# Optimization experiments

Measured on AMD Instinct MI355X. Metric: run time of the kernel, lower is better.

The kernel has to match this reference:

```python
import jax, jax.numpy as jnp
import numpy as np

N_COMBIN, N_DEV, CONT, VOCAB, EMB = 50000, 100000, 62, 1000, 16
B, K, H, OUT, NCLS = 8192, 64, 4, 16, 1
FEAT = CONT + 2 * EMB  # 94
ALPHA = 0.2  # leaky relu slope


def setup_inputs() -> dict:
    key = jax.random.key(0)
    ks = jax.random.split(key, 32)
    rn = lambda k, shape, s=0.05: (jax.random.normal(k, shape, dtype=jnp.float32) * s)
    inp = {
        "combin_cont": jax.random.normal(ks[0], (N_COMBIN, CONT), jnp.float32),
        "combin_cat": jax.random.randint(ks[1], (N_COMBIN, 2), 0, VOCAB),
        "device_cont": jax.random.normal(ks[2], (N_DEV, CONT), jnp.float32),
        "device_cat": jax.random.randint(ks[3], (N_DEV, 2), 0, VOCAB),
        "combin_idx": jax.random.randint(ks[4], (B,), 0, N_COMBIN),
        "device_idx": jax.random.randint(ks[5], (B,), 0, N_DEV),
        "neighbor_idx": jax.random.randint(ks[6], (B, K), 0, N_DEV),
        "ce0": rn(ks[7], (VOCAB, EMB), 1.0),
        "ce1": rn(ks[8], (VOCAB, EMB), 1.0),
        "de0": rn(ks[9], (VOCAB, EMB), 1.0),
        "de1": rn(ks[10], (VOCAB, EMB), 1.0),
        "Wc": rn(ks[11], (H, FEAT, OUT)),
        "bc": rn(ks[12], (H, OUT)),
        "Wd": rn(ks[13], (H, FEAT, OUT)),
        "bd": rn(ks[14], (H, OUT)),
        "aW": rn(ks[15], (H, 2 * OUT)),
        "ab": rn(ks[16], (H,)),
        "W1": rn(ks[17], (H * OUT, OUT)),
        "b1": rn(ks[18], (OUT,)),
        "W2": rn(ks[19], (OUT + 2 * FEAT, 64)),
        "b2": rn(ks[20], (64,)),
        "W3": rn(ks[21], (64, 32)),
        "b3": rn(ks[22], (32,)),
        "W4": rn(ks[23], (32, NCLS)),
        "b4": rn(ks[24], (NCLS,)),
    }
    return inp


def reference(combin_cont, combin_cat, device_cont, device_cat,
              combin_idx, device_idx, neighbor_idx,
              ce0, ce1, de0, de1,
              Wc, bc, Wd, bd, aW, ab,
              W1, b1, W2, b2, W3, b3, W4, b4):
    # concat_embed_feats for device nodes: [N_dev, FEAT]
    dev_feats = jnp.concatenate(
        [device_cont, de0[device_cat[:, 0]], de1[device_cat[:, 1]]], axis=1)
    # combin batch features: [B, FEAT]
    cc = combin_cat[combin_idx]
    comb_batch = jnp.concatenate(
        [combin_cont[combin_idx], ce0[cc[:, 0]], ce1[cc[:, 1]]], axis=1)
    dev_batch = dev_feats[device_idx]            # [B, FEAT]
    neibr = dev_feats[neighbor_idx]              # [B, K, FEAT]

    # multi-head GAT attention (all heads vectorized)
    h_c = jnp.einsum('bf,hfo->bho', comb_batch, Wc) + bc[None]          # [B,H,OUT]
    h_n = jnp.einsum('bkf,hfo->bhko', neibr, Wd) + bd[None, :, None]    # [B,H,K,OUT]
    a1, a2 = aW[:, :OUT], aW[:, OUT:]
    e = (jnp.einsum('bho,ho->bh', h_c, a1)[:, :, None]
         + jnp.einsum('bhko,ho->bhk', h_n, a2)
         + ab[None, :, None])                                           # [B,H,K]
    e = jax.nn.leaky_relu(e, negative_slope=ALPHA)
    attn = jax.nn.softmax(e, axis=-1)
    head_out = jax.nn.elu(jnp.einsum('bhk,bhko->bho', attn, h_n))       # [B,H,OUT]
    attn_feats = head_out.reshape(head_out.shape[0], H * OUT) @ W1 + b1  # [B,OUT]

    fusion = jnp.concatenate([comb_batch, dev_batch, attn_feats], axis=1)
    x = jax.nn.relu(fusion @ W2 + b2)   # dropout is identity in eval
    x = jax.nn.relu(x @ W3 + b3)
    return jax.nn.sigmoid(x @ W4 + b4)  # [B, NCLS]
```

## Files before the change

kernel.cpp:

```cpp
#include <hip/hip_runtime.h>
#include <cmath>

#define NDEV   100000
#define NBATCH 8192
#define CONTF  62
#define EMB    16
#define FEAT   94
#define KNBR   64
#define NH     4
#define OUTD   16
#define HOUT   64
#define FUS    204
#define ALPHA  0.2f

#define NDEVG2  782
#define NCOMBG2 64
#define KP      48
#define WROWS   68

typedef unsigned short ushortT;
typedef unsigned int   uintT;
typedef ushortT ushort8v __attribute__((ext_vector_type(8)));
typedef short   short8  __attribute__((ext_vector_type(8)));
typedef float   float4v __attribute__((ext_vector_type(4)));


template <typename T>
__device__ __forceinline__ const T* uniform_ptr(const T* p) {
  uint64_t v = (uint64_t)(uintptr_t)p;
  uint32_t lo = __builtin_amdgcn_readfirstlane((uint32_t)v);
  uint32_t hi = __builtin_amdgcn_readfirstlane((uint32_t)(v >> 32));
  return (const T*)(uintptr_t)(((uint64_t)hi << 32) | lo);
}

__device__ __forceinline__ float bf2f(ushortT u) {
  return __uint_as_float(((unsigned int)u) << 16);
}
__device__ __forceinline__ ushortT f2bf(float f) {
  unsigned int i = __float_as_uint(f);
  unsigned int r = i + 0x7FFFu + ((i >> 16) & 1u);
  return (ushortT)(r >> 16);
}
__device__ __forceinline__ uintT pack2(float lo, float hi) {
  return ((uintT)f2bf(hi) << 16) | (uintT)f2bf(lo);
}

union FragU { uint4 u; short8 s; };

__global__ __launch_bounds__(256) void k_prep(
    const float* __restrict__ Wd, const float* __restrict__ Wc,
    const float* __restrict__ aW,
    uintT* __restrict__ wpack) {
  const int e = blockIdx.x * 256 + threadIdx.x;
  if (e >= 2 * WROWS * KP) return;
  const bool dev = e < WROWS * KP;
  const int i = dev ? e : e - WROWS * KP;
  const int n = i / KP, p = i - n * KP;
  const float* __restrict__ Ws = dev ? Wd : Wc;
  uintT v = 0u;
  if (p < 47) {
    if (n < 64) {
      const int h = n >> 4, o = n & 15;
      const float lo = Ws[(h * FEAT + 2 * p) * OUTD + o];
      const float hi = Ws[(h * FEAT + 2 * p + 1) * OUTD + o];
      v = pack2(lo, hi);
    } else {
      const int hd = n - 64;
      const float* __restrict__ av = aW + hd * 2 * OUTD + (dev ? OUTD : 0);
      float lo = 0.f, hi = 0.f;
#pragma unroll
      for (int o = 0; o < OUTD; ++o) {
        lo = fmaf(Ws[(hd * FEAT + 2 * p) * OUTD + o], av[o], lo);
        hi = fmaf(Ws[(hd * FEAT + 2 * p + 1) * OUTD + o], av[o], hi);
      }
      v = pack2(lo, hi);
    }
  }
  wpack[e] = v;
}

__global__ __launch_bounds__(256, 2) void k_feat(
    const float* __restrict__ device_cont, const int* __restrict__ device_cat,
    const float* __restrict__ de0, const float* __restrict__ de1,
    const float* __restrict__ bd,
    const float* __restrict__ combin_cont, const int* __restrict__ combin_cat,
    const int* __restrict__ combin_idx,
    const float* __restrict__ ce0, const float* __restrict__ ce1,
    const float* __restrict__ bc,
    const float* __restrict__ aW, const uintT* __restrict__ wpack,
    ushortT* __restrict__ h_bf, float* __restrict__ e_d, float* __restrict__ e_c) {
  __shared__ uintT x_s[128 * KP];
  __shared__ uintT w_s[80 * KP];
  __shared__ int   ci_s[128];

  const int tid  = threadIdx.x;
  const int lane = tid & 63;
  const int wv = __builtin_amdgcn_readfirstlane((int)(tid >> 6));
  const int blk = blockIdx.x;
  const bool devp = blk < NDEVG2;
  const int b0 = (devp ? blk : blk - NDEVG2) * 128;

  if (!devp && tid < 128) ci_s[tid] = combin_idx[b0 + tid];

  {
    const uint4* __restrict__ wp =
        reinterpret_cast<const uint4*>(wpack + (devp ? 0 : WROWS * KP));
    uint4* __restrict__ ws4 = reinterpret_cast<uint4*>(w_s);
#pragma unroll
    for (int t = 0; t < 4; ++t) {
      const int idx = t * 256 + tid;
      if (idx < 960)
        ws4[idx] = (idx < 816) ? wp[idx] : make_uint4(0u, 0u, 0u, 0u);
    }
  }
  __syncthreads();

  {
    const float* __restrict__ cont = devp ? device_cont : combin_cont;
#pragma unroll 1
    for (int e = tid; e < 128 * 31; e += 256) {
      const int r = e / 31, p = e - r * 31;
      const size_t srow = devp ? (size_t)min(b0 + r, NDEV - 1) : (size_t)ci_s[r];
      const float2 v = *reinterpret_cast<const float2*>(cont + srow * CONTF + 2 * p);
      x_s[r * KP + p] = pack2(v.x, v.y);
    }
  }
  {
    const int r = tid >> 1, tb = tid & 1;
    const int srow = devp ? min(b0 + r, NDEV - 1) : ci_s[r];
    const int cidx = (devp ? device_cat : combin_cat)[2 * srow + tb];
    const float* __restrict__ ep =
        (tb ? (devp ? de1 : ce1) : (devp ? de0 : ce0)) + (size_t)cidx * EMB;
    uintT* __restrict__ dst = &x_s[r * KP + 31 + tb * 8];
#pragma unroll
    for (int k4 = 0; k4 < 4; ++k4) {
      const float4 v = reinterpret_cast<const float4*>(ep)[k4];
      dst[2 * k4 + 0] = pack2(v.x, v.y);
      dst[2 * k4 + 1] = pack2(v.z, v.w);
    }
  }
  if (tid < 128) x_s[tid * KP + 47] = 0u;
  __syncthreads();

  const int m = lane & 15, q = lane >> 4;
  const int aoff = devp ? OUTD : 0;
  const float* bias = uniform_ptr(devp ? bd : bc);
  const float* aWl  = uniform_ptr(aW);

  float4v acc[2][NH];
#pragma unroll
  for (int ct = 0; ct < NH; ++ct) {
    const float bv = bias[ct * OUTD + m];
    acc[0][ct] = (float4v){bv, bv, bv, bv};
    acc[1][ct] = (float4v){bv, bv, bv, bv};
  }
  float bec = 0.f;
  if (m < NH) {
    const float* __restrict__ av = aWl + m * 2 * OUTD + aoff;
#pragma unroll
    for (int o = 0; o < OUTD; ++o) bec = fmaf(bias[m * OUTD + o], av[o], bec);
  }
  float4v acc_e[2];
  acc_e[0] = (float4v){bec, bec, bec, bec};
  acc_e[1] = (float4v){bec, bec, bec, bec};

  const uintT* xa0 = &x_s[(wv * 16 + m) * KP + q * 4];
  const uintT* xa1 = &x_s[(64 + wv * 16 + m) * KP + q * 4];
#pragma unroll
  for (int c = 0; c < 3; ++c) {
    FragU af0, af1;
    af0.u = *reinterpret_cast<const uint4*>(xa0 + c * 16);
    af1.u = *reinterpret_cast<const uint4*>(xa1 + c * 16);
#pragma unroll
    for (int ct = 0; ct < NH; ++ct) {
      FragU bf;
      bf.u = *reinterpret_cast<const uint4*>(&w_s[(ct * 16 + m) * KP + c * 16 + q * 4]);
      acc[0][ct] = __builtin_amdgcn_mfma_f32_16x16x32_bf16(af0.s, bf.s, acc[0][ct], 0, 0, 0);
      acc[1][ct] = __builtin_amdgcn_mfma_f32_16x16x32_bf16(af1.s, bf.s, acc[1][ct], 0, 0, 0);
    }
    FragU bfe;
    bfe.u = *reinterpret_cast<const uint4*>(&w_s[(64 + m) * KP + c * 16 + q * 4]);
    acc_e[0] = __builtin_amdgcn_mfma_f32_16x16x32_bf16(af0.s, bfe.s, acc_e[0], 0, 0, 0);
    acc_e[1] = __builtin_amdgcn_mfma_f32_16x16x32_bf16(af1.s, bfe.s, acc_e[1], 0, 0, 0);
  }

  float* __restrict__ eout = devp ? e_d : e_c;
#pragma unroll
  for (int rt = 0; rt < 2; ++rt) {
    const int rowq = b0 + rt * 64 + wv * 16 + q * 4;
    if (m < NH) {
#pragma unroll
      for (int r = 0; r < 4; ++r)
        if (!devp || rowq + r < NDEV) eout[(size_t)(rowq + r) * NH + m] = acc_e[rt][r];
    }
    if (devp) {
#pragma unroll
      for (int ct = 0; ct < NH; ++ct) {
#pragma unroll
        for (int r = 0; r < 4; ++r) {
          if (rowq + r < NDEV)
            h_bf[(size_t)(rowq + r) * HOUT + ct * OUTD + m] = f2bf(acc[rt][ct][r]);
        }
      }
    }
  }
}

__global__ __launch_bounds__(256, 4) void k_attn(
    const int* __restrict__ neighbor_idx, const int* __restrict__ device_idx,
    const int* __restrict__ device_cat, const float* __restrict__ device_cont,
    const float* __restrict__ de0, const float* __restrict__ de1,
    const int* __restrict__ combin_idx, const int* __restrict__ combin_cat,
    const float* __restrict__ combin_cont,
    const float* __restrict__ ce0, const float* __restrict__ ce1,
    const ushortT* __restrict__ h_bf, const float* __restrict__ e_d,
    const float* __restrict__ e_c, const float* __restrict__ ab,
    const float* __restrict__ W1, const float* __restrict__ b1,
    const float* __restrict__ W2, const float* __restrict__ b2,
    const float* __restrict__ W3, const float* __restrict__ b3,
    const float* __restrict__ W4, const float* __restrict__ b4,
    float* __restrict__ out) {
  __shared__ __align__(16) float pb[4][NH][68];
  __shared__ __align__(16) float hb[4][HOUT];
  __shared__ __align__(16) float fusb[4][208];
  __shared__ __align__(16) float x1b[4][64];

  const int lane = threadIdx.x & 63;
  const int wid  = __builtin_amdgcn_readfirstlane((int)(threadIdx.x >> 6));
  const int b    = blockIdx.x * 4 + wid;

  const int nk = neighbor_idx[(size_t)b * KNBR + lane];
  const float4 ed4 = *reinterpret_cast<const float4*>(e_d + (size_t)nk * NH);
  const float4 ec4 = *reinterpret_cast<const float4*>(e_c + (size_t)b * NH);
  const float4 ab4 = *reinterpret_cast<const float4*>(ab);

  const int q = lane >> 3, c8 = lane & 7;
  ushort8v hpre[8];
#pragma unroll
  for (int t = 0; t < 8; ++t) {
    const int nt = __shfl(nk, q * 8 + t);
    hpre[t] = *reinterpret_cast<const ushort8v*>(h_bf + (size_t)nt * HOUT + c8 * 8);
  }

  const int ci = combin_idx[b];
  const int cc0 = combin_cat[2 * ci], cc1 = combin_cat[2 * ci + 1];
  const int didx = device_idx[b];
  const int dc0 = device_cat[2 * didx], dc1 = device_cat[2 * didx + 1];
#pragma unroll
  for (int t = 0; t < 3; ++t) {
    const int i = lane + t * 64;
    if (i < 188) {
      float v;
      if (i < 62)       v = combin_cont[(size_t)ci * CONTF + i];
      else if (i < 78)  v = ce0[(size_t)cc0 * EMB + (i - 62)];
      else if (i < 94)  v = ce1[(size_t)cc1 * EMB + (i - 78)];
      else if (i < 156) v = device_cont[(size_t)didx * CONTF + (i - 94)];
      else if (i < 172) v = de0[(size_t)dc0 * EMB + (i - 156)];
      else              v = de1[(size_t)dc1 * EMB + (i - 172)];
      fusb[wid][i] = v;
    }
  }

  float v0 = ec4.x + ed4.x + ab4.x;
  float v1 = ec4.y + ed4.y + ab4.y;
  float v2 = ec4.z + ed4.z + ab4.z;
  float v3 = ec4.w + ed4.w + ab4.w;
  v0 = v0 > 0.f ? v0 : ALPHA * v0;
  v1 = v1 > 0.f ? v1 : ALPHA * v1;
  v2 = v2 > 0.f ? v2 : ALPHA * v2;
  v3 = v3 > 0.f ? v3 : ALPHA * v3;

  float p0 = expf(v0), p1 = expf(v1), p2 = expf(v2), p3 = expf(v3);
  float s0 = p0, s1 = p1, s2 = p2, s3 = p3;
#pragma unroll
  for (int msk = 1; msk < 64; msk <<= 1) {
    s0 += __shfl_xor(s0, msk);
    s1 += __shfl_xor(s1, msk);
    s2 += __shfl_xor(s2, msk);
    s3 += __shfl_xor(s3, msk);
  }
  p0 /= s0; p1 /= s1; p2 /= s2; p3 /= s3;

  pb[wid][0][lane] = p0;
  pb[wid][1][lane] = p1;
  pb[wid][2][lane] = p2;
  pb[wid][3][lane] = p3;
  __builtin_amdgcn_wave_barrier();

  {
    const int hq = c8 >> 1;
    const float4 pA4 = *reinterpret_cast<const float4*>(&pb[wid][hq][q * 8]);
    const float4 pB4 = *reinterpret_cast<const float4*>(&pb[wid][hq][q * 8 + 4]);
    const float pv[8] = {pA4.x, pA4.y, pA4.z, pA4.w,
                         pB4.x, pB4.y, pB4.z, pB4.w};
    float a[8];
#pragma unroll
    for (int i = 0; i < 8; ++i) a[i] = 0.f;
#pragma unroll
    for (int t = 0; t < 8; ++t) {
      const float p = pv[t];
#pragma unroll
      for (int i = 0; i < 8; ++i) a[i] = fmaf(p, bf2f(hpre[t][i]), a[i]);
    }
#pragma unroll
    for (int msk = 8; msk < 64; msk <<= 1) {
#pragma unroll
      for (int i = 0; i < 8; ++i) a[i] += __shfl_xor(a[i], msk);
    }
    if (q == 0) {
#pragma unroll
      for (int i = 0; i < 8; ++i) a[i] = a[i] > 0.f ? a[i] : expm1f(a[i]);
      float4* hp = reinterpret_cast<float4*>(&hb[wid][c8 * 8]);
      hp[0] = make_float4(a[0], a[1], a[2], a[3]);
      hp[1] = make_float4(a[4], a[5], a[6], a[7]);
    }
  }
  __builtin_amdgcn_wave_barrier();

  {
    const int j = lane & 15, gg = lane >> 4;
    const float4* hv4 = reinterpret_cast<const float4*>(&hb[wid][gg * 16]);
    float pc0 = 0.f, pc1 = 0.f;
#pragma unroll
    for (int t4 = 0; t4 < 4; ++t4) {
      const float4 hv = hv4[t4];
      const int tb = gg * 16 + t4 * 4;
      pc0 = fmaf(hv.x, W1[(tb + 0) * OUTD + j], pc0);
      pc1 = fmaf(hv.y, W1[(tb + 1) * OUTD + j], pc1);
      pc0 = fmaf(hv.z, W1[(tb + 2) * OUTD + j], pc0);
      pc1 = fmaf(hv.w, W1[(tb + 3) * OUTD + j], pc1);
    }
    float part = pc0 + pc1;
    part += __shfl_xor(part, 16);
    part += __shfl_xor(part, 32);
    if (lane < 16) fusb[wid][188 + lane] = part + b1[lane];
  }
  __builtin_amdgcn_wave_barrier();

  {
    float a0 = b2[lane], a1 = 0.f, a2 = 0.f, a3 = 0.f;
    const float4* fu4 = reinterpret_cast<const float4*>(fusb[wid]);
#pragma unroll 3
    for (int f4 = 0; f4 < 51; ++f4) {
      const float4 u = fu4[f4];
      const int fb = f4 * 4;
      a0 = fmaf(u.x, W2[(fb + 0) * 64 + lane], a0);
      a1 = fmaf(u.y, W2[(fb + 1) * 64 + lane], a1);
      a2 = fmaf(u.z, W2[(fb + 2) * 64 + lane], a2);
      a3 = fmaf(u.w, W2[(fb + 3) * 64 + lane], a3);
    }
    x1b[wid][lane] = fmaxf((a0 + a1) + (a2 + a3), 0.f);
  }
  __builtin_amdgcn_wave_barrier();

  const int m = lane & 31, rh = lane >> 5;
  {
    float x2a = rh ? 0.f : b3[m], x2b = 0.f, x2c = 0.f, x2d = 0.f;
    const float4* xv4 = reinterpret_cast<const float4*>(&x1b[wid][rh * 32]);
#pragma unroll
    for (int j4 = 0; j4 < 8; ++j4) {
      const float4 xv = xv4[j4];
      const int jb = rh * 32 + j4 * 4;
      x2a = fmaf(xv.x, W3[(jb + 0) * 32 + m], x2a);
      x2b = fmaf(xv.y, W3[(jb + 1) * 32 + m], x2b);
      x2c = fmaf(xv.z, W3[(jb + 2) * 32 + m], x2c);
      x2d = fmaf(xv.w, W3[(jb + 3) * 32 + m], x2d);
    }
    float x2 = (x2a + x2b) + (x2c + x2d);
    x2 += __shfl_xor(x2, 32);
    float pL3 = fmaxf(x2, 0.f) * W4[m];
#pragma unroll
    for (int msk = 1; msk < 32; msk <<= 1) pL3 += __shfl_xor(pL3, msk);
    if (lane == 0) {
      const float z = pL3 + b4[0];
      out[b] = 1.f / (1.f + expf(-z));
    }
  }
}

extern "C" void kernel_launch(void* const* d_in, const int* in_sizes, int n_in,
                              void* d_out, int out_size, void* d_ws, size_t ws_size,
                              hipStream_t stream) {
  const float* combin_cont  = (const float*)d_in[0];
  const int*   combin_cat   = (const int*)d_in[1];
  const float* device_cont  = (const float*)d_in[2];
  const int*   device_cat   = (const int*)d_in[3];
  const int*   combin_idx   = (const int*)d_in[4];
  const int*   device_idx   = (const int*)d_in[5];
  const int*   neighbor_idx = (const int*)d_in[6];
  const float* ce0 = (const float*)d_in[7];
  const float* ce1 = (const float*)d_in[8];
  const float* de0 = (const float*)d_in[9];
  const float* de1 = (const float*)d_in[10];
  const float* Wc  = (const float*)d_in[11];
  const float* bc  = (const float*)d_in[12];
  const float* Wd  = (const float*)d_in[13];
  const float* bd  = (const float*)d_in[14];
  const float* aW  = (const float*)d_in[15];
  const float* ab  = (const float*)d_in[16];
  const float* W1  = (const float*)d_in[17];
  const float* b1  = (const float*)d_in[18];
  const float* W2  = (const float*)d_in[19];
  const float* b2  = (const float*)d_in[20];
  const float* W3  = (const float*)d_in[21];
  const float* b3  = (const float*)d_in[22];
  const float* W4  = (const float*)d_in[23];
  const float* b4  = (const float*)d_in[24];

  float* ws  = (float*)d_ws;
  ushortT* h_bf = (ushortT*)ws;
  float* e_d = ws + 3200000;
  float* e_c = ws + 3600000;
  uintT* wpack = (uintT*)(ws + 3632768);

  k_prep<<<26, 256, 0, stream>>>(Wd, Wc, aW, wpack);
  k_feat<<<NDEVG2 + NCOMBG2, 256, 0, stream>>>(
      device_cont, device_cat, de0, de1, bd,
      combin_cont, combin_cat, combin_idx, ce0, ce1, bc, aW, wpack,
      h_bf, e_d, e_c);
  k_attn<<<2048, 256, 0, stream>>>(
      neighbor_idx, device_idx, device_cat, device_cont, de0, de1,
      combin_idx, combin_cat, combin_cont, ce0, ce1,
      h_bf, e_d, e_c, ab, W1, b1, W2, b2, W3, b3, W4, b4, (float*)d_out);
}
```

Baseline: 162.2 us.

## Process two batch rows per wave in attention kernel; skip unused combin h MFMAs

The attention/MLP kernel now has each wave handle two batch rows instead of one. Weight loads for W1, W2 and W3 are shared across both rows, and the neighbor h gathers for both rows are issued together to raise memory-level parallelism. The grid is halved to match. Separately, the feature kernel skips the per-head h MFMAs for combin blocks, which only need the attention-score column. The cost is doubled register pressure from two hpre arrays, which could reduce occupancy under launch_bounds(256,4).

```diff
diff --git a/kernel.cpp b/kernel.cpp
--- a/kernel.cpp
+++ b/kernel.cpp
@@ -148,11 +148,13 @@
   const float* aWl  = uniform_ptr(aW);
 
   float4v acc[2][NH];
-#pragma unroll
-  for (int ct = 0; ct < NH; ++ct) {
-    const float bv = bias[ct * OUTD + m];
-    acc[0][ct] = (float4v){bv, bv, bv, bv};
-    acc[1][ct] = (float4v){bv, bv, bv, bv};
+  if (devp) {
+#pragma unroll
+    for (int ct = 0; ct < NH; ++ct) {
+      const float bv = bias[ct * OUTD + m];
+      acc[0][ct] = (float4v){bv, bv, bv, bv};
+      acc[1][ct] = (float4v){bv, bv, bv, bv};
+    }
   }
   float bec = 0.f;
   if (m < NH) {
@@ -171,12 +173,14 @@
     FragU af0, af1;
     af0.u = *reinterpret_cast<const uint4*>(xa0 + c * 16);
     af1.u = *reinterpret_cast<const uint4*>(xa1 + c * 16);
-#pragma unroll
-    for (int ct = 0; ct < NH; ++ct) {
-      FragU bf;
-      bf.u = *reinterpret_cast<const uint4*>(&w_s[(ct * 16 + m) * KP + c * 16 + q * 4]);
-      acc[0][ct] = __builtin_amdgcn_mfma_f32_16x16x32_bf16(af0.s, bf.s, acc[0][ct], 0, 0, 0);
-      acc[1][ct] = __builtin_amdgcn_mfma_f32_16x16x32_bf16(af1.s, bf.s, acc[1][ct], 0, 0, 0);
+    if (devp) {
+#pragma unroll
+      for (int ct = 0; ct < NH; ++ct) {
+        FragU bf;
+        bf.u = *reinterpret_cast<const uint4*>(&w_s[(ct * 16 + m) * KP + c * 16 + q * 4]);
+        acc[0][ct] = __builtin_amdgcn_mfma_f32_16x16x32_bf16(af0.s, bf.s, acc[0][ct], 0, 0, 0);
+        acc[1][ct] = __builtin_amdgcn_mfma_f32_16x16x32_bf16(af1.s, bf.s, acc[1][ct], 0, 0, 0);
+      }
     }
     FragU bfe;
     bfe.u = *reinterpret_cast<const uint4*>(&w_s[(64 + m) * KP + c * 16 + q * 4]);
@@ -220,160 +224,223 @@
     const float* __restrict__ W3, const float* __restrict__ b3,
     const float* __restrict__ W4, const float* __restrict__ b4,
     float* __restrict__ out) {
-  __shared__ __align__(16) float pb[4][NH][68];
-  __shared__ __align__(16) float hb[4][HOUT];
-  __shared__ __align__(16) float fusb[4][208];
-  __shared__ __align__(16) float x1b[4][64];
+  __shared__ __align__(16) float pb[8][NH][68];
+  __shared__ __align__(16) float hb[8][HOUT];
+  __shared__ __align__(16) float fusb[8][208];
+  __shared__ __align__(16) float x1b[8][64];
 
   const int lane = threadIdx.x & 63;
   const int wid  = __builtin_amdgcn_readfirstlane((int)(threadIdx.x >> 6));
-  const int b    = blockIdx.x * 4 + wid;
-
-  const int nk = neighbor_idx[(size_t)b * KNBR + lane];
-  const float4 ed4 = *reinterpret_cast<const float4*>(e_d + (size_t)nk * NH);
-  const float4 ec4 = *reinterpret_cast<const float4*>(e_c + (size_t)b * NH);
-  const float4 ab4 = *reinterpret_cast<const float4*>(ab);
+  const int row0 = blockIdx.x * 8 + wid * 2;
+  const int row1 = row0 + 1;
+  const int rl0  = wid * 2, rl1 = rl0 + 1;
+
+  const int nk0 = neighbor_idx[(size_t)row0 * KNBR + lane];
+  const int nk1 = neighbor_idx[(size_t)row1 * KNBR + lane];
+  const float4 ed40 = *reinterpret_cast<const float4*>(e_d + (size_t)nk0 * NH);
+  const float4 ed41 = *reinterpret_cast<const float4*>(e_d + (size_t)nk1 * NH);
+  const float4 ec40 = *reinterpret_cast<const float4*>(e_c + (size_t)row0 * NH);
+  const float4 ec41 = *reinterpret_cast<const float4*>(e_c + (size_t)row1 * NH);
+  const float4 ab4  = *reinterpret_cast<const float4*>(ab);
 
   const int q = lane >> 3, c8 = lane & 7;
-  ushort8v hpre[8];
+  ushort8v hpre0[8], hpre1[8];
 #pragma unroll
   for (int t = 0; t < 8; ++t) {
-    const int nt = __shfl(nk, q * 8 + t);
-    hpre[t] = *reinterpret_cast<const ushort8v*>(h_bf + (size_t)nt * HOUT + c8 * 8);
-  }
-
-  const int ci = combin_idx[b];
-  const int cc0 = combin_cat[2 * ci], cc1 = combin_cat[2 * ci + 1];
-  const int didx = device_idx[b];
-  const int dc0 = device_cat[2 * didx], dc1 = device_cat[2 * didx + 1];
-#pragma unroll
-  for (int t = 0; t < 3; ++t) {
-    const int i = lane + t * 64;
-    if (i < 188) {
-      float v;
-      if (i < 62)       v = combin_cont[(size_t)ci * CONTF + i];
-      else if (i < 78)  v = ce0[(size_t)cc0 * EMB + (i - 62)];
-      else if (i < 94)  v = ce1[(size_t)cc1 * EMB + (i - 78)];
-      else if (i < 156) v = device_cont[(size_t)didx * CONTF + (i - 94)];
-      else if (i < 172) v = de0[(size_t)dc0 * EMB + (i - 156)];
-      else              v = de1[(size_t)dc1 * EMB + (i - 172)];
-      fusb[wid][i] = v;
-    }
-  }
-
-  float v0 = ec4.x + ed4.x + ab4.x;
-  float v1 = ec4.y + ed4.y + ab4.y;
-  float v2 = ec4.z + ed4.z + ab4.z;
-  float v3 = ec4.w + ed4.w + ab4.w;
-  v0 = v0 > 0.f ? v0 : ALPHA * v0;
-  v1 = v1 > 0.f ? v1 : ALPHA * v1;
-  v2 = v2 > 0.f ? v2 : ALPHA * v2;
-  v3 = v3 > 0.f ? v3 : ALPHA * v3;
-
-  float p0 = expf(v0), p1 = expf(v1), p2 = expf(v2), p3 = expf(v3);
-  float s0 = p0, s1 = p1, s2 = p2, s3 = p3;
-#pragma unroll
-  for (int msk = 1; msk < 64; msk <<= 1) {
-    s0 += __shfl_xor(s0, msk);
-    s1 += __shfl_xor(s1, msk);
-    s2 += __shfl_xor(s2, msk);
-    s3 += __shfl_xor(s3, msk);
-  }
-  p0 /= s0; p1 /= s1; p2 /= s2; p3 /= s3;
-
-  pb[wid][0][lane] = p0;
-  pb[wid][1][lane] = p1;
-  pb[wid][2][lane] = p2;
-  pb[wid][3][lane] = p3;
+    const int nt0 = __shfl(nk0, q * 8 + t);
+    const int nt1 = __shfl(nk1, q * 8 + t);
+    hpre0[t] = *reinterpret_cast<const ushort8v*>(h_bf + (size_t)nt0 * HOUT + c8 * 8);
+    hpre1[t] = *reinterpret_cast<const ushort8v*>(h_bf + (size_t)nt1 * HOUT + c8 * 8);
+  }
+
+#pragma unroll
+  for (int r2 = 0; r2 < 2; ++r2) {
+    const int bb_ = r2 ? row1 : row0;
+    const int rl  = r2 ? rl1 : rl0;
+    const int ci = combin_idx[bb_];
+    const int cc0 = combin_cat[2 * ci], cc1 = combin_cat[2 * ci + 1];
+    const int didx = device_idx[bb_];
+    const int dc0 = device_cat[2 * didx], dc1 = device_cat[2 * didx + 1];
+#pragma unroll
+    for (int t = 0; t < 3; ++t) {
+      const int i = lane + t * 64;
+      if (i < 188) {
+        float v;
+        if (i < 62)       v = combin_cont[(size_t)ci * CONTF + i];
+        else if (i < 78)  v = ce0[(size_t)cc0 * EMB + (i - 62)];
+        else if (i < 94)  v = ce1[(size_t)cc1 * EMB + (i - 78)];
+        else if (i < 156) v = device_cont[(size_t)didx * CONTF + (i - 94)];
+        else if (i < 172) v = de0[(size_t)dc0 * EMB + (i - 156)];
+        else              v = de1[(size_t)dc1 * EMB + (i - 172)];
+        fusb[rl][i] = v;
+      }
+    }
+  }
+
+  {
+    float u0 = ec40.x + ed40.x + ab4.x;
+    float u1 = ec40.y + ed40.y + ab4.y;
+    float u2 = ec40.z + ed40.z + ab4.z;
+    float u3 = ec40.w + ed40.w + ab4.w;
+    float w0 = ec41.x + ed41.x + ab4.x;
+    float w1 = ec41.y + ed41.y + ab4.y;
+    float w2 = ec41.z + ed41.z + ab4.z;
+    float w3 = ec41.w + ed41.w + ab4.w;
+    u0 = u0 > 0.f ? u0 : ALPHA * u0;  u1 = u1 > 0.f ? u1 : ALPHA * u1;
+    u2 = u2 > 0.f ? u2 : ALPHA * u2;  u3 = u3 > 0.f ? u3 : ALPHA * u3;
+    w0 = w0 > 0.f ? w0 : ALPHA * w0;  w1 = w1 > 0.f ? w1 : ALPHA * w1;
+    w2 = w2 > 0.f ? w2 : ALPHA * w2;  w3 = w3 > 0.f ? w3 : ALPHA * w3;
+
+    float p00 = expf(u0), p01 = expf(u1), p02 = expf(u2), p03 = expf(u3);
+    float p10 = expf(w0), p11 = expf(w1), p12 = expf(w2), p13 = expf(w3);
+    float s00 = p00, s01 = p01, s02 = p02, s03 = p03;
+    float s10 = p10, s11 = p11, s12 = p12, s13 = p13;
+#pragma unroll
+    for (int msk = 1; msk < 64; msk <<= 1) {
+      s00 += __shfl_xor(s00, msk);  s01 += __shfl_xor(s01, msk);
+      s02 += __shfl_xor(s02, msk);  s03 += __shfl_xor(s03, msk);
+      s10 += __shfl_xor(s10, msk);  s11 += __shfl_xor(s11, msk);
+      s12 += __shfl_xor(s12, msk);  s13 += __shfl_xor(s13, msk);
+    }
+    pb[rl0][0][lane] = p00 / s00;
+    pb[rl0][1][lane] = p01 / s01;
+    pb[rl0][2][lane] = p02 / s02;
+    pb[rl0][3][lane] = p03 / s03;
+    pb[rl1][0][lane] = p10 / s10;
+    pb[rl1][1][lane] = p11 / s11;
+    pb[rl1][2][lane] = p12 / s12;
+    pb[rl1][3][lane] = p13 / s13;
+  }
   __builtin_amdgcn_wave_barrier();
 
   {
     const int hq = c8 >> 1;
-    const float4 pA4 = *reinterpret_cast<const float4*>(&pb[wid][hq][q * 8]);
-    const float4 pB4 = *reinterpret_cast<const float4*>(&pb[wid][hq][q * 8 + 4]);
-    const float pv[8] = {pA4.x, pA4.y, pA4.z, pA4.w,
-                         pB4.x, pB4.y, pB4.z, pB4.w};
-    float a[8];
-#pragma unroll
-    for (int i = 0; i < 8; ++i) a[i] = 0.f;
-#pragma unroll
-    for (int t = 0; t < 8; ++t) {
-      const float p = pv[t];
-#pragma unroll
-      for (int i = 0; i < 8; ++i) a[i] = fmaf(p, bf2f(hpre[t][i]), a[i]);
-    }
-#pragma unroll
-    for (int msk = 8; msk < 64; msk <<= 1) {
-#pragma unroll
-      for (int i = 0; i < 8; ++i) a[i] += __shfl_xor(a[i], msk);
-    }
-    if (q == 0) {
-#pragma unroll
-      for (int i = 0; i < 8; ++i) a[i] = a[i] > 0.f ? a[i] : expm1f(a[i]);
-      float4* hp = reinterpret_cast<float4*>(&hb[wid][c8 * 8]);
-      hp[0] = make_float4(a[0], a[1], a[2], a[3]);
-      hp[1] = make_float4(a[4], a[5], a[6], a[7]);
+#pragma unroll
+    for (int r2 = 0; r2 < 2; ++r2) {
+      const int rl = r2 ? rl1 : rl0;
+      const float4 pA4 = *reinterpret_cast<const float4*>(&pb[rl][hq][q * 8]);
+      const float4 pB4 = *reinterpret_cast<const float4*>(&pb[rl][hq][q * 8 + 4]);
+      const float pv[8] = {pA4.x, pA4.y, pA4.z, pA4.w,
+                           pB4.x, pB4.y, pB4.z, pB4.w};
+      float a[8];
+#pragma unroll
+      for (int i = 0; i < 8; ++i) a[i] = 0.f;
+#pragma unroll
+      for (int t = 0; t < 8; ++t) {
+        const float p = pv[t];
+        const ushort8v hv = r2 ? hpre1[t] : hpre0[t];
+#pragma unroll
+        for (int i = 0; i < 8; ++i) a[i] = fmaf(p, bf2f(hv[i]), a[i]);
+      }
+#pragma unroll
+      for (int msk = 8; msk < 64; msk <<= 1) {
+#pragma unroll
+        for (int i = 0; i < 8; ++i) a[i] += __shfl_xor(a[i], msk);
+      }
+      if (q == 0) {
+#pragma unroll
+        for (int i = 0; i < 8; ++i) a[i] = a[i] > 0.f ? a[i] : expm1f(a[i]);
+        float4* hp = reinterpret_cast<float4*>(&hb[rl][c8 * 8]);
+        hp[0] = make_float4(a[0], a[1], a[2], a[3]);
+        hp[1] = make_float4(a[4], a[5], a[6], a[7]);
+      }
     }
   }
   __builtin_amdgcn_wave_barrier();
 
   {
     const int j = lane & 15, gg = lane >> 4;
-    const float4* hv4 = reinterpret_cast<const float4*>(&hb[wid][gg * 16]);
-    float pc0 = 0.f, pc1 = 0.f;
+    const float4* hv40 = reinterpret_cast<const float4*>(&hb[rl0][gg * 16]);
+    const float4* hv41 = reinterpret_cast<const float4*>(&hb[rl1][gg * 16]);
+    float pa0 = 0.f, pa1 = 0.f, pb0_ = 0.f, pb1_ = 0.f;
 #pragma unroll
     for (int t4 = 0; t4 < 4; ++t4) {
-      const float4 hv = hv4[t4];
+      const float4 h0 = hv40[t4];
+      const float4 h1 = hv41[t4];
       const int tb = gg * 16 + t4 * 4;
-      pc0 = fmaf(hv.x, W1[(tb + 0) * OUTD + j], pc0);
-      pc1 = fmaf(hv.y, W1[(tb + 1) * OUTD + j], pc1);
-      pc0 = fmaf(hv.z, W1[(tb + 2) * OUTD + j], pc0);
-      pc1 = fmaf(hv.w, W1[(tb + 3) * OUTD + j], pc1);
-    }
-    float part = pc0 + pc1;
-    part += __shfl_xor(part, 16);
-    part += __shfl_xor(part, 32);
-    if (lane < 16) fusb[wid][188 + lane] = part + b1[lane];
+      const float wA = W1[(tb + 0) * OUTD + j];
+      const float wB = W1[(tb + 1) * OUTD + j];
+      const float wC = W1[(tb + 2) * OUTD + j];
+      const float wD = W1[(tb + 3) * OUTD + j];
+      pa0 = fmaf(h0.x, wA, pa0);  pb0_ = fmaf(h1.x, wA, pb0_);
+      pa1 = fmaf(h0.y, wB, pa1);  pb1_ = fmaf(h1.y, wB, pb1_);
+      pa0 = fmaf(h0.z, wC, pa0);  pb0_ = fmaf(h1.z, wC, pb0_);
+      pa1 = fmaf(h0.w, wD, pa1);  pb1_ = fmaf(h1.w, wD, pb1_);
+    }
+    float part0 = pa0 + pa1;
+    float part1 = pb0_ + pb1_;
+    part0 += __shfl_xor(part0, 16);
+    part0 += __shfl_xor(part0, 32);
+    part1 += __shfl_xor(part1, 16);
+    part1 += __shfl_xor(part1, 32);
+    if (lane < 16) {
+      const float bb = b1[lane];
+      fusb[rl0][188 + lane] = part0 + bb;
+      fusb[rl1][188 + lane] = part1 + bb;
+    }
   }
   __builtin_amdgcn_wave_barrier();
 
   {
-    float a0 = b2[lane], a1 = 0.f, a2 = 0.f, a3 = 0.f;
-    const float4* fu4 = reinterpret_cast<const float4*>(fusb[wid]);
+    float a00 = b2[lane], a01 = 0.f, a02 = 0.f, a03 = 0.f;
+    float a10 = a00,      a11 = 0.f, a12 = 0.f, a13 = 0.f;
+    const float4* fu40 = reinterpret_cast<const float4*>(fusb[rl0]);
+    const float4* fu41 = reinterpret_cast<const float4*>(fusb[rl1]);
 #pragma unroll 3
     for (int f4 = 0; f4 < 51; ++f4) {
-      const float4 u = fu4[f4];
+      const float4 u0 = fu40[f4];
+      const float4 u1 = fu41[f4];
       const int fb = f4 * 4;
-      a0 = fmaf(u.x, W2[(fb + 0) * 64 + lane], a0);
-      a1 = fmaf(u.y, W2[(fb + 1) * 64 + lane], a1);
-      a2 = fmaf(u.z, W2[(fb + 2) * 64 + lane], a2);
-      a3 = fmaf(u.w, W2[(fb + 3) * 64 + lane], a3);
-    }
-    x1b[wid][lane] = fmaxf((a0 + a1) + (a2 + a3), 0.f);
+      const float wA = W2[(fb + 0) * 64 + lane];
+      const float wB = W2[(fb + 1) * 64 + lane];
+      const float wC = W2[(fb + 2) * 64 + lane];
+      const float wD = W2[(fb + 3) * 64 + lane];
+      a00 = fmaf(u0.x, wA, a00);  a10 = fmaf(u1.x, wA, a10);
+      a01 = fmaf(u0.y, wB, a01);  a11 = fmaf(u1.y, wB, a11);
+      a02 = fmaf(u0.z, wC, a02);  a12 = fmaf(u1.z, wC, a12);
+      a03 = fmaf(u0.w, wD, a03);  a13 = fmaf(u1.w, wD, a13);
+    }
+    x1b[rl0][lane] = fmaxf((a00 + a01) + (a02 + a03), 0.f);
+    x1b[rl1][lane] = fmaxf((a10 + a11) + (a12 + a13), 0.f);
   }
   __builtin_amdgcn_wave_barrier();
 
   const int m = lane & 31, rh = lane >> 5;
   {
-    float x2a = rh ? 0.f : b3[m], x2b = 0.f, x2c = 0.f, x2d = 0.f;
-    const float4* xv4 = reinterpret_cast<const float4*>(&x1b[wid][rh * 32]);
+    float xa0 = rh ? 0.f : b3[m], xa1 = 0.f, xa2 = 0.f, xa3 = 0.f;
+    float xb0 = rh ? 0.f : b3[m], xb1 = 0.f, xb2 = 0.f, xb3 = 0.f;
+    const float4* xv40 = reinterpret_cast<const float4*>(&x1b[rl0][rh * 32]);
+    const float4* xv41 = reinterpret_cast<const float4*>(&x1b[rl1][rh * 32]);
 #pragma unroll
     for (int j4 = 0; j4 < 8; ++j4) {
-      const float4 xv = xv4[j4];
+      const float4 x0 = xv40[j4];
+      const float4 x1 = xv41[j4];
       const int jb = rh * 32 + j4 * 4;
-      x2a = fmaf(xv.x, W3[(jb + 0) * 32 + m], x2a);
-      x2b = fmaf(xv.y, W3[(jb + 1) * 32 + m], x2b);
-      x2c = fmaf(xv.z, W3[(jb + 2) * 32 + m], x2c);
-      x2d = fmaf(xv.w, W3[(jb + 3) * 32 + m], x2d);
-    }
-    float x2 = (x2a + x2b) + (x2c + x2d);
-    x2 += __shfl_xor(x2, 32);
-    float pL3 = fmaxf(x2, 0.f) * W4[m];
-#pragma unroll
-    for (int msk = 1; msk < 32; msk <<= 1) pL3 += __shfl_xor(pL3, msk);
+      const float wA = W3[(jb + 0) * 32 + m];
+      const float wB = W3[(jb + 1) * 32 + m];
+      const float wC = W3[(jb + 2) * 32 + m];
+      const float wD = W3[(jb + 3) * 32 + m];
+      xa0 = fmaf(x0.x, wA, xa0);  xb0 = fmaf(x1.x, wA, xb0);
+      xa1 = fmaf(x0.y, wB, xa1);  xb1 = fmaf(x1.y, wB, xb1);
+      xa2 = fmaf(x0.z, wC, xa2);  xb2 = fmaf(x1.z, wC, xb2);
+      xa3 = fmaf(x0.w, wD, xa3);  xb3 = fmaf(x1.w, wD, xb3);
+    }
+    float x20 = (xa0 + xa1) + (xa2 + xa3);
+    float x21 = (xb0 + xb1) + (xb2 + xb3);
+    x20 += __shfl_xor(x20, 32);
+    x21 += __shfl_xor(x21, 32);
+    const float w4 = W4[m];
+    float pL0 = fmaxf(x20, 0.f) * w4;
+    float pL1 = fmaxf(x21, 0.f) * w4;
+#pragma unroll
+    for (int msk = 1; msk < 32; msk <<= 1) {
+      pL0 += __shfl_xor(pL0, msk);
+      pL1 += __shfl_xor(pL1, msk);
+    }
     if (lane == 0) {
-      const float z = pL3 + b4[0];
-      out[b] = 1.f / (1.f + expf(-z));
+      const float bz = b4[0];
+      out[row0] = 1.f / (1.f + expf(-(pL0 + bz)));
+      out[row1] = 1.f / (1.f + expf(-(pL1 + bz)));
     }
   }
 }
@@ -418,7 +485,7 @@
       device_cont, device_cat, de0, de1, bd,
       combin_cont, combin_cat, combin_idx, ce0, ce1, bc, aW, wpack,
       h_bf, e_d, e_c);
-  k_attn<<<2048, 256, 0, stream>>>(
+  k_attn<<<NBATCH / 8, 256, 0, stream>>>(
       neighbor_idx, device_idx, device_cat, device_cont, de0, de1,
       combin_idx, combin_cat, combin_cont, ce0, ce1,
       h_bf, e_d, e_c, ab, W1, b1, W2, b2, W3, b3, W4, b4, (float*)d_out);
```

New measurement: 161.9 us. Within noise of the previous version (-0.2%).
